# Kernel tuning notes

Measured on AMD Instinct MI355X. Metric: run time of the kernel, lower is better.

Reference implementation:

```python
import jax, jax.numpy as jnp
import numpy as np

B, N, D = 512, 120, 64
NB = 8  # n_freq_bands
S_CLIP, DELTA_CLIP = 10.0, 5.0


def zc_rms(x, g, eps=1e-8):
    # zero-centred RMS norm
    x0 = x - x0_mean(x)
    return x0 * jax.lax.rsqrt(jnp.mean(x0 * x0, axis=-1, keepdims=True) + eps) * g


def x0_mean(x):
    return jnp.mean(x, axis=-1, keepdims=True)


def l2norm(x, eps=1e-8):
    return x * jax.lax.rsqrt(jnp.sum(x * x, axis=-1, keepdims=True) + eps)


def setup_inputs() -> dict:
    key = jax.random.key(0)
    ks = jax.random.split(key, 12)
    s = 1.0 / np.sqrt(D)
    return {
        "x": jax.random.normal(ks[0], (B, N, D), dtype=jnp.float32),
        "g_norm": jnp.ones((D,), jnp.float32),
        "Wq": jax.random.normal(ks[1], (D, D), jnp.float32) * s,
        "Wk": jax.random.normal(ks[2], (D, D), jnp.float32) * s,
        "Wv": jax.random.normal(ks[3], (D, D), jnp.float32) * s,
        "bv": jnp.zeros((D,), jnp.float32),
        "Wo": jax.random.normal(ks[4], (D, D), jnp.float32) * s,
        "bo": jnp.zeros((D,), jnp.float32),
        "g_post": jnp.ones((D,), jnp.float32),
        "W1": jax.random.normal(ks[5], (NB, 16), jnp.float32) * (1.0 / np.sqrt(NB)),
        "b1": jnp.zeros((16,), jnp.float32),
        "W2": jax.random.normal(ks[6], (16, 1), jnp.float32) * 0.25,
        "b2": jnp.full((1,), 0.5, jnp.float32),  # bias init 0.5 as in torch
    }


def _gamma(h, W1, b1, W2, b2):
    # FFT over embedding dim, band-averaged energies -> gate in [0.5, 0.99]
    fft = jnp.abs(jnp.fft.rfft(jax.lax.stop_gradient(h), axis=-1))  # (B,N,n_f)
    n_f = fft.shape[-1]
    bs = max(1, n_f // NB)
    bands = [fft[..., i * bs:min(i * bs + bs, n_f)].mean(-1) for i in range(NB)]
    energy = jnp.stack(bands, axis=-1)  # (B,N,NB)
    energy = energy / jnp.clip(jnp.sum(energy, axis=-1, keepdims=True), 1e-8)
    hdn = jax.nn.silu(energy @ W1 + b1)
    raw = jax.nn.sigmoid(hdn @ W2 + b2)  # (B,N,1)
    return 0.5 + 0.49 * raw


def reference(x, g_norm, Wq, Wk, Wv, bv, Wo, bo, g_post, W1, b1, W2, b2):
    h = zc_rms(x, g_norm)
    q = l2norm(h @ Wq)
    k = l2norm(h @ Wk)
    v = h @ Wv + bv
    gamma = _gamma(h, W1, b1, W2, b2)  # (B,N,1)

    # time-major for scan
    qT = jnp.moveaxis(q, 1, 0)      # (N,B,D)
    kT = jnp.moveaxis(k, 1, 0)
    vT = jnp.moveaxis(v, 1, 0)
    gT = jnp.moveaxis(gamma, 1, 0)  # (N,B,1)

    S0 = jnp.zeros((x.shape[0], D, D), x.dtype)

    def step(S, inp):
        q_t, k_t, v_t, g_t = inp
        pred = jnp.einsum('bde,be->bd', S, k_t)
        delta = jnp.clip(v_t - pred, -DELTA_CLIP, DELTA_CLIP)
        S = g_t[..., None] * S + delta[:, :, None] * k_t[:, None, :]
        S = jnp.clip(S, -S_CLIP, S_CLIP)
        o_t = jnp.einsum('bde,be->bd', S, q_t)
        return S, o_t

    _, outT = jax.lax.scan(step, S0, (qT, kT, vT, gT))
    out = jnp.moveaxis(outT, 0, 1)  # (B,N,D)
    out = zc_rms(out, g_post) @ Wo + bo  # dropout is identity at inference
    return x + out
```

## Files before the change

kernel.cpp:

```cpp
#include <hip/hip_runtime.h>
#include <math.h>

#define B_ 512
#define N_ 120

typedef __attribute__((ext_vector_type(8))) _Float16 f16x8;
typedef __attribute__((ext_vector_type(2))) _Float16 f16x2;
typedef __attribute__((ext_vector_type(4))) float f32x4;
typedef __attribute__((ext_vector_type(2))) float f32x2;
typedef __attribute__((ext_vector_type(4))) int i32x4;

#define DPP_XOR1 0xB1
#define DPP_XOR2 0x4E
#define DPP_HMIR 0x141
#define DPP_MIR  0x140
template<int CTRL>
__device__ __forceinline__ float dpp_add(float v) {
    int x = __builtin_amdgcn_mov_dpp(__float_as_int(v), CTRL, 0xF, 0xF, true);
    return v + __int_as_float(x);
}

__device__ __forceinline__ float mix_lo(float a, int b, float c) {
    float d;
    asm("v_fma_mix_f32 %0, %1, %2, %3 op_sel:[0,0,0] op_sel_hi:[0,1,0]"
        : "=v"(d) : "v"(a), "v"(b), "v"(c));
    return d;
}
__device__ __forceinline__ float mix_hi(float a, int b, float c) {
    float d;
    asm("v_fma_mix_f32 %0, %1, %2, %3 op_sel:[0,1,0] op_sel_hi:[0,1,0]"
        : "=v"(d) : "v"(a), "v"(b), "v"(c));
    return d;
}
__device__ __forceinline__ f32x2 pk_mul2(f32x2 a, f32x2 b) {
    f32x2 d;
    asm("v_pk_mul_f32 %0, %1, %2" : "=v"(d) : "v"(a), "v"(b));
    return d;
}

#define OFF_WQ 0
#define OFF_WK 4096
#define OFF_WV 8192
#define OFF_T  12288
#define OFF_XF 16384
#define OFF_QS 0
#define OFF_KS 7680
#define OFF_VS 15360
#define OFF_OF 23040
#define OFF_WO 31232
#define LDS_F16 35328

__device__ __forceinline__ void mm4(f16x8 a0, f16x8 a1, const _Float16* wmat,
                                    int lane, f32x4* acc) {
    const f16x8* wv = (const f16x8*)wmat;
    #pragma unroll
    for (int nt = 0; nt < 4; ++nt) {
        f32x4 z = {0.f, 0.f, 0.f, 0.f};
        z = __builtin_amdgcn_mfma_f32_16x16x32_f16(a0, wv[nt * 128 + lane], z, 0, 0, 0);
        z = __builtin_amdgcn_mfma_f32_16x16x32_f16(a1, wv[nt * 128 + 64 + lane], z, 0, 0, 0);
        acc[nt] = z;
    }
}

__global__ __launch_bounds__(512, 4) void fused_kdn(
    const float* __restrict__ x, const float* __restrict__ g_norm,
    const float* __restrict__ Wq, const float* __restrict__ Wk,
    const float* __restrict__ Wv, const float* __restrict__ bv,
    const float* __restrict__ Wo, const float* __restrict__ bo,
    const float* __restrict__ g_post,
    const float* __restrict__ W1, const float* __restrict__ b1,
    const float* __restrict__ W2, const float* __restrict__ b2,
    float* out)
{
    __shared__ __align__(16) _Float16 L[LDS_F16];
    __shared__ __align__(16) float g_s[N_];
    __shared__ float bv_s[64], bo_s[64];
    __shared__ float sW1[128], sb1[16], sW2[16], sb2_s[1];

    int tid = threadIdx.x, wave = tid >> 6, lane = tid & 63;
    int b = blockIdx.x;

    if (tid < 128) sW1[tid] = W1[tid];
    if (tid >= 128 && tid < 144) sb1[tid - 128] = b1[tid - 128];
    if (tid >= 144 && tid < 160) sW2[tid - 144] = W2[tid - 144];
    if (tid == 160) sb2_s[0] = b2[0];
    if (tid >= 192 && tid < 256) bv_s[tid - 192] = bv[tid - 192];
    if (tid >= 256 && tid < 320) bo_s[tid - 256] = bo[tid - 256];
    if (tid < 128) {
        f16x8 z = {0, 0, 0, 0, 0, 0, 0, 0};
        *(f16x8*)&L[OFF_XF + 7168 + tid * 8] = z;
        *(f16x8*)&L[OFF_OF + 7168 + tid * 8] = z;
    }
    int sn = tid & 63, sk0 = (tid >> 6) * 8;
    int widx = (sn >> 4) * 1024 + (sk0 >> 5) * 512 + ((((sk0 >> 3) & 3) << 4) + (sn & 15)) * 8;
    {
        const float* Ws[4] = { Wq, Wk, Wv, Wo };
        const int woff[4] = { OFF_WQ, OFF_WK, OFF_WV, OFF_WO };
        #pragma unroll
        for (int m = 0; m < 4; ++m) {
            f16x8 pv;
            #pragma unroll
            for (int j = 0; j < 8; ++j) pv[j] = (_Float16)Ws[m][(sk0 + j) * 64 + sn];
            *(f16x8*)&L[woff[m] + widx] = pv;
        }
        f16x8 pv;
        int nn = sn & 31;
        #pragma unroll
        for (int j = 0; j < 8; ++j) {
            int kk = ((sk0 + j) * nn) & 63;
            float a = (float)kk * (6.283185307179586f / 64.0f);
            float s, c; __sincosf(a, &s, &c);
            pv[j] = (_Float16)((sn < 32) ? c : s);
        }
        *(f16x8*)&L[OFF_T + widx] = pv;
    }
    __syncthreads();

    const float* xb = x + (size_t)b * N_ * 64;
    float* ob_g = out + (size_t)b * N_ * 64;

    {
        float gn = g_norm[lane];
        int hbase = (lane >> 5) * 512 + ((lane >> 3) & 3) * 128 + (lane & 7);
        #pragma unroll 5
        for (int c = 0; c < 15; ++c) {
            int row = wave * 15 + c;
            float xv = xb[row * 64 + lane];
            float sx = xv, sxx = xv * xv;
            sx = dpp_add<DPP_XOR1>(sx); sxx = dpp_add<DPP_XOR1>(sxx);
            sx = dpp_add<DPP_XOR2>(sx); sxx = dpp_add<DPP_XOR2>(sxx);
            sx = dpp_add<DPP_HMIR>(sx); sxx = dpp_add<DPP_HMIR>(sxx);
            sx = dpp_add<DPP_MIR >(sx); sxx = dpp_add<DPP_MIR >(sxx);
            sx += __shfl_xor(sx, 16);   sxx += __shfl_xor(sxx, 16);
            sx += __shfl_xor(sx, 32);   sxx += __shfl_xor(sxx, 32);
            float mean = sx * 0.015625f;
            float var  = sxx * 0.015625f - mean * mean;
            float h = (xv - mean) * rsqrtf(var + 1e-8f) * gn;
            float hp = __shfl_xor(h, 1);
            if (!(lane & 1)) {
                f16x2 pk2 = { (_Float16)h, (_Float16)hp };
                *(f16x2*)&L[OFF_XF + (row >> 4) * 1024 + (row & 15) * 8 + hbase] = pk2;
            }
        }
    }
    __syncthreads();

    int grp = lane >> 4, li = lane & 15;
    int rbase = wave * 16 + grp * 4;
    {
        const f16x8* hfv = (const f16x8*)(L + OFF_XF);
        f16x8 a0 = hfv[wave * 128 + lane];
        f16x8 a1 = hfv[wave * 128 + 64 + lane];
        f32x4 accT[4];

        mm4(a0, a1, L + OFF_T, lane, accT);
        {
            int gb2 = lane & 48;
            #pragma unroll
            for (int reg = 0; reg < 4; ++reg) {
                float re1 = accT[0][reg], re2 = accT[1][reg];
                float im1 = accT[2][reg], im2 = accT[3][reg];
                float m1 = sqrtf(fmaf(re1, re1, im1 * im1));
                float m2 = sqrtf(fmaf(re2, re2, im2 * im2));
                m1 = dpp_add<DPP_XOR1>(m1); m2 = dpp_add<DPP_XOR1>(m2);
                m1 = dpp_add<DPP_XOR2>(m1); m2 = dpp_add<DPP_XOR2>(m2);
                float e1 = m1 * 0.25f, e2 = m2 * 0.25f;
                float tot = e1 + e2;
                tot = dpp_add<DPP_HMIR>(tot);
                tot = dpp_add<DPP_MIR >(tot);
                float rinv = 1.0f / fmaxf(tot, 1e-8f);
                float en1 = e1 * rinv, en2 = e2 * rinv;
                float hs = sb1[li];
                #pragma unroll
                for (int i = 0; i < 4; ++i)
                    hs = fmaf(__shfl(en1, gb2 + (i << 2)), sW1[i * 16 + li], hs);
                #pragma unroll
                for (int i = 0; i < 4; ++i)
                    hs = fmaf(__shfl(en2, gb2 + (i << 2)), sW1[(i + 4) * 16 + li], hs);
                float act = hs / (1.0f + __expf(-hs));
                float p = act * sW2[li];
                p = dpp_add<DPP_XOR1>(p);
                p = dpp_add<DPP_XOR2>(p);
                p = dpp_add<DPP_HMIR>(p);
                p = dpp_add<DPP_MIR >(p);
                float raw = 1.0f / (1.0f + __expf(-(p + sb2_s[0])));
                int row = rbase + reg;
                if (li == 0 && row < N_) g_s[row] = fmaf(0.49f, raw, 0.5f);
            }
        }

        f32x4 accq[4], acck[4], accv[4];
        mm4(a0, a1, L + OFF_WQ, lane, accq);
        mm4(a0, a1, L + OFF_WK, lane, acck);
        mm4(a0, a1, L + OFF_WV, lane, accv);

        {
            f32x4 sq = accq[0]*accq[0] + accq[1]*accq[1] + accq[2]*accq[2] + accq[3]*accq[3];
            f32x4 sk = acck[0]*acck[0] + acck[1]*acck[1] + acck[2]*acck[2] + acck[3]*acck[3];
            #pragma unroll
            for (int reg = 0; reg < 4; ++reg) {
                float qs = sq[reg], ks = sk[reg];
                qs = dpp_add<DPP_XOR1>(qs); ks = dpp_add<DPP_XOR1>(ks);
                qs = dpp_add<DPP_XOR2>(qs); ks = dpp_add<DPP_XOR2>(ks);
                qs = dpp_add<DPP_HMIR>(qs); ks = dpp_add<DPP_HMIR>(ks);
                qs = dpp_add<DPP_MIR >(qs); ks = dpp_add<DPP_MIR >(ks);
                float rq = rsqrtf(qs + 1e-8f), rk = rsqrtf(ks + 1e-8f);
                #pragma unroll
                for (int nt = 0; nt < 4; ++nt) { accq[nt][reg] *= rq; acck[nt][reg] *= rk; }
            }
            #pragma unroll
            for (int nt = 0; nt < 4; ++nt) {
                float bvn = bv_s[nt * 16 + li];
                #pragma unroll
                for (int reg = 0; reg < 4; ++reg) accv[nt][reg] += bvn;
            }
        }
        __syncthreads();

        #pragma unroll
        for (int reg = 0; reg < 4; ++reg) {
            int row = rbase + reg;
            if (row < N_) {
                int base = row * 64 + li;
                #pragma unroll
                for (int nt = 0; nt < 4; ++nt) {
                    L[OFF_QS + base + nt * 16] = (_Float16)accq[nt][reg];
                    L[OFF_KS + base + nt * 16] = (_Float16)acck[nt][reg];
                    L[OFF_VS + base + nt * 16] = (_Float16)accv[nt][reg];
                }
            }
        }
    }
    __syncthreads();

    {
        int g8 = lane & 7, dlo = lane >> 3;
        int d = wave * 8 + dlo;
        int co = g8 * 8;
        int dbase = (d >> 5) * 512 + ((d >> 3) & 3) * 128 + (d & 7);
        const _Float16* ks = L + OFF_KS;
        const _Float16* qs = L + OFF_QS;
        const _Float16* vp = L + OFF_VS + d;

        f32x2 S2[4];
        #pragma unroll
        for (int j = 0; j < 4; ++j) { S2[j].x = 0.f; S2[j].y = 0.f; }

        f16x8 kh = *(const f16x8*)&ks[co];
        f16x8 qh = *(const f16x8*)&qs[co];
        _Float16 vh = vp[0];
        f16x8 kn = *(const f16x8*)&ks[64 + co];
        f16x8 qn = *(const f16x8*)&qs[64 + co];
        _Float16 vn = vp[64];
        float pbc = 0.f;
        float4 gq = *(const float4*)&g_s[0];

#define PAIR(j, kh2, qh2, kn2) {                                               \
            f32x2 t2 = pk_mul2(gt2, S2[j]);                                    \
            float sA = mix_lo(delta, kh2, t2.x);                               \
            float sB = mix_hi(delta, kh2, t2.y);                               \
            sA = __builtin_amdgcn_fmed3f(sA, -10.f, 10.f);                     \
            sB = __builtin_amdgcn_fmed3f(sB, -10.f, 10.f);                     \
            S2[j].x = sA; S2[j].y = sB;                                        \
            oa = mix_lo(sA, qh2, oa);  ob = mix_hi(sB, qh2, ob);               \
            pa = mix_lo(sA, kn2, pa);  pb = mix_hi(sB, kn2, pb); }

#define SCAN_STEP(T, TF, GT)                                                   \
        {                                                                      \
            f16x8 kf = *(const f16x8*)&ks[(TF) * 64 + co];                     \
            f16x8 qf = *(const f16x8*)&qs[(TF) * 64 + co];                     \
            _Float16 vf = vp[(TF) * 64];                                       \
            float gt = (GT);                                                   \
            f32x2 gt2; gt2.x = gt; gt2.y = gt;                                 \
            float delta = __builtin_amdgcn_fmed3f((float)vh - pbc, -5.0f, 5.0f);\
            i32x4 khi = *(i32x4*)&kh;                                          \
            i32x4 qhi = *(i32x4*)&qh;                                          \
            i32x4 kni = *(i32x4*)&kn;                                          \
            float oa = 0.f, ob = 0.f, pa = 0.f, pb = 0.f;                      \
            PAIR(0, khi[0], qhi[0], kni[0])                                    \
            PAIR(1, khi[1], qhi[1], kni[1])                                    \
            PAIR(2, khi[2], qhi[2], kni[2])                                    \
            PAIR(3, khi[3], qhi[3], kni[3])                                    \
            float o = oa + ob;                                                 \
            o = dpp_add<DPP_XOR1>(o);                                          \
            o = dpp_add<DPP_XOR2>(o);                                          \
            o = dpp_add<DPP_HMIR>(o);                                          \
            float pn = pa + pb;                                                \
            pn = dpp_add<DPP_XOR1>(pn);                                        \
            pn = dpp_add<DPP_XOR2>(pn);                                        \
            pn = dpp_add<DPP_HMIR>(pn);                                        \
            if (g8 == 0)                                                       \
                L[OFF_OF + ((T) >> 4) * 1024 + ((T) & 15) * 8 + dbase] = (_Float16)o; \
            pbc = pn;                                                          \
            kh = kn; qh = qn; vh = vn;                                         \
            kn = kf; qn = qf; vn = vf;                                         \
        }

        for (int t4 = 0; t4 < 116; t4 += 4) {
            float4 gq_n = *(const float4*)&g_s[t4 + 4];
            SCAN_STEP(t4 + 0, t4 + 2, gq.x)
            SCAN_STEP(t4 + 1, t4 + 3, gq.y)
            SCAN_STEP(t4 + 2, t4 + 4, gq.z)
            SCAN_STEP(t4 + 3, t4 + 5, gq.w)
            gq = gq_n;
        }
        SCAN_STEP(116, 118, gq.x)
        SCAN_STEP(117, 119, gq.y)
        SCAN_STEP(118, 119, gq.z)
        SCAN_STEP(119, 119, gq.w)
#undef SCAN_STEP
#undef PAIR
    }
    __syncthreads();

    {
        float gp = g_post[lane];
        int hbase = (lane >> 5) * 512 + ((lane >> 3) & 3) * 128 + (lane & 7);
        #pragma unroll 5
        for (int c = 0; c < 15; ++c) {
            int row = wave * 15 + c;
            int ridx = OFF_OF + (row >> 4) * 1024 + (row & 15) * 8;
            float ov = (float)L[ridx + hbase];
            float sx = ov, sxx = ov * ov;
            sx = dpp_add<DPP_XOR1>(sx); sxx = dpp_add<DPP_XOR1>(sxx);
            sx = dpp_add<DPP_XOR2>(sx); sxx = dpp_add<DPP_XOR2>(sxx);
            sx = dpp_add<DPP_HMIR>(sx); sxx = dpp_add<DPP_HMIR>(sxx);
            sx = dpp_add<DPP_MIR >(sx); sxx = dpp_add<DPP_MIR >(sxx);
            sx += __shfl_xor(sx, 16);   sxx += __shfl_xor(sxx, 16);
            sx += __shfl_xor(sx, 32);   sxx += __shfl_xor(sxx, 32);
            float mean = sx * 0.015625f;
            float var  = sxx * 0.015625f - mean * mean;
            float hn = (ov - mean) * rsqrtf(var + 1e-8f) * gp;
            float hp = __shfl_xor(hn, 1);
            if (!(lane & 1)) {
                f16x2 pk2 = { (_Float16)hn, (_Float16)hp };
                *(f16x2*)&L[ridx + hbase] = pk2;
            }
        }
    }
    __syncthreads();

    {
        const f16x8* hfv = (const f16x8*)(L + OFF_OF);
        f16x8 a0 = hfv[wave * 128 + lane];
        f16x8 a1 = hfv[wave * 128 + 64 + lane];
        f32x4 acc[4];
        mm4(a0, a1, L + OFF_WO, lane, acc);
        #pragma unroll
        for (int reg = 0; reg < 4; ++reg) {
            int row = rbase + reg;
            if (row < N_) {
                #pragma unroll
                for (int nt = 0; nt < 4; ++nt) {
                    int idx = row * 64 + nt * 16 + li;
                    ob_g[idx] = acc[nt][reg] + bo_s[nt * 16 + li] + xb[idx];
                }
            }
        }
    }
}

extern "C" void kernel_launch(void* const* d_in, const int* in_sizes, int n_in,
                              void* d_out, int out_size, void* d_ws, size_t ws_size,
                              hipStream_t stream)
{
    const float* x      = (const float*)d_in[0];
    const float* g_norm = (const float*)d_in[1];
    const float* Wq     = (const float*)d_in[2];
    const float* Wk     = (const float*)d_in[3];
    const float* Wv     = (const float*)d_in[4];
    const float* bv     = (const float*)d_in[5];
    const float* Wo     = (const float*)d_in[6];
    const float* bo     = (const float*)d_in[7];
    const float* g_post = (const float*)d_in[8];
    const float* W1     = (const float*)d_in[9];
    const float* b1     = (const float*)d_in[10];
    const float* W2     = (const float*)d_in[11];
    const float* b2     = (const float*)d_in[12];
    float* out = (float*)d_out;

    fused_kdn<<<B_, 512, 0, stream>>>(x, g_norm, Wq, Wk, Wv, bv, Wo, bo, g_post,
                                      W1, b1, W2, b2, out);
}
```

Measured before the change: 157.8 us.

## Compute scan state-vector products with MFMA on four waves

The recurrent scan is restructured so the per-step matrix-vector products (S·q for the output and S·k_next for the next prediction) run as 16x16x32 MFMA instructions instead of per-lane mixed-precision FMAs followed by DPP reductions. The updated state is packed to fp16 each step and used as the A operand, with column 0 of B holding q and column 1 holding the next k. Only four waves run the scan, and deltas are exchanged through a small LDS scratch each step. This removes the cross-lane reduction chains but adds an LDS round-trip and MFMA latency on the serial critical path, halves scan parallelism, and rounds S to fp16 before the products.

```diff
diff --git a/kernel.cpp b/kernel.cpp
--- a/kernel.cpp
+++ b/kernel.cpp
@@ -36,6 +36,10 @@
     f32x2 d;
     asm("v_pk_mul_f32 %0, %1, %2" : "=v"(d) : "v"(a), "v"(b));
     return d;
+}
+__device__ __forceinline__ int pkrtz_i32(float a, float b) {
+    auto sp = __builtin_amdgcn_cvt_pkrtz(a, b);
+    return *(int*)&sp;
 }
 
 #define OFF_WQ 0
@@ -74,6 +78,7 @@
 {
     __shared__ __align__(16) _Float16 L[LDS_F16];
     __shared__ __align__(16) float g_s[N_];
+    __shared__ __align__(16) float dsc[4][16];
     __shared__ float bv_s[64], bo_s[64];
     __shared__ float sW1[128], sb1[16], sW2[16], sb2_s[1];
 
@@ -233,83 +238,83 @@
     }
     __syncthreads();
 
-    {
-        int g8 = lane & 7, dlo = lane >> 3;
-        int d = wave * 8 + dlo;
-        int co = g8 * 8;
-        int dbase = (d >> 5) * 512 + ((d >> 3) & 3) * 128 + (d & 7);
-        const _Float16* ks = L + OFF_KS;
-        const _Float16* qs = L + OFF_QS;
-        const _Float16* vp = L + OFF_VS + d;
-
-        f32x2 S2[4];
-        #pragma unroll
-        for (int j = 0; j < 4; ++j) { S2[j].x = 0.f; S2[j].y = 0.f; }
-
-        f16x8 kh = *(const f16x8*)&ks[co];
-        f16x8 qh = *(const f16x8*)&qs[co];
-        _Float16 vh = vp[0];
-        f16x8 kn = *(const f16x8*)&ks[64 + co];
-        f16x8 qn = *(const f16x8*)&qs[64 + co];
-        _Float16 vn = vp[64];
-        float pbc = 0.f;
+    if (wave < 4) {
+        int col = lane & 15;
+        int kg  = lane >> 4;
+        int c0  = kg * 8;
+        int d0  = wave * 16 + kg * 4;
+        int dpart = (d0 >> 5) * 512 + ((d0 >> 3) & 3) * 128 + (d0 & 7);
+        const _Float16* ksp = L + OFF_KS;
+        const _Float16* qsp = L + OFF_QS;
+        const _Float16* vsp = L + OFF_VS;
+        const _Float16* bbase = (col == 1) ? (ksp + 64 + c0) : (qsp + c0);
+
+        f32x2 S2[8];
+        #pragma unroll
+        for (int j = 0; j < 8; ++j) { S2[j].x = 0.f; S2[j].y = 0.f; }
+        f32x4 ppC = {0.f, 0.f, 0.f, 0.f};
+        const float fone = 1.0f, fzero = 0.0f;
         float4 gq = *(const float4*)&g_s[0];
 
-#define PAIR(j, kh2, qh2, kn2) {                                               \
+#define UPD2(j, KW, DST)                                                       \
+        {                                                                      \
             f32x2 t2 = pk_mul2(gt2, S2[j]);                                    \
-            float sA = mix_lo(delta, kh2, t2.x);                               \
-            float sB = mix_hi(delta, kh2, t2.y);                               \
-            sA = __builtin_amdgcn_fmed3f(sA, -10.f, 10.f);                     \
-            sB = __builtin_amdgcn_fmed3f(sB, -10.f, 10.f);                     \
-            S2[j].x = sA; S2[j].y = sB;                                        \
-            oa = mix_lo(sA, qh2, oa);  ob = mix_hi(sB, qh2, ob);               \
-            pa = mix_lo(sA, kn2, pa);  pb = mix_hi(sB, kn2, pb); }
-
-#define SCAN_STEP(T, TF, GT)                                                   \
+            float sa = mix_lo(delta, KW, t2.x);                                \
+            float sb = mix_hi(delta, KW, t2.y);                                \
+            sa = __builtin_amdgcn_fmed3f(sa, -10.f, 10.f);                     \
+            sb = __builtin_amdgcn_fmed3f(sb, -10.f, 10.f);                     \
+            S2[j].x = sa; S2[j].y = sb;                                        \
+            DST = pkrtz_i32(sa, sb);                                           \
+        }
+
+#define SCAN_IT(T, GT)                                                         \
         {                                                                      \
-            f16x8 kf = *(const f16x8*)&ks[(TF) * 64 + co];                     \
-            f16x8 qf = *(const f16x8*)&qs[(TF) * 64 + co];                     \
-            _Float16 vf = vp[(TF) * 64];                                       \
+            int2  vw  = *(const int2 *)&vsp[(T) * 64 + d0];                    \
+            f16x8 ku0 = *(const f16x8*)&ksp[(T) * 64 + c0];                    \
+            f16x8 ku1 = *(const f16x8*)&ksp[(T) * 64 + c0 + 32];               \
+            f16x8 b0  = *(const f16x8*)&bbase[(T) * 64];                       \
+            f16x8 b1  = *(const f16x8*)&bbase[(T) * 64 + 32];                  \
             float gt = (GT);                                                   \
             f32x2 gt2; gt2.x = gt; gt2.y = gt;                                 \
-            float delta = __builtin_amdgcn_fmed3f((float)vh - pbc, -5.0f, 5.0f);\
-            i32x4 khi = *(i32x4*)&kh;                                          \
-            i32x4 qhi = *(i32x4*)&qh;                                          \
-            i32x4 kni = *(i32x4*)&kn;                                          \
-            float oa = 0.f, ob = 0.f, pa = 0.f, pb = 0.f;                      \
-            PAIR(0, khi[0], qhi[0], kni[0])                                    \
-            PAIR(1, khi[1], qhi[1], kni[1])                                    \
-            PAIR(2, khi[2], qhi[2], kni[2])                                    \
-            PAIR(3, khi[3], qhi[3], kni[3])                                    \
-            float o = oa + ob;                                                 \
-            o = dpp_add<DPP_XOR1>(o);                                          \
-            o = dpp_add<DPP_XOR2>(o);                                          \
-            o = dpp_add<DPP_HMIR>(o);                                          \
-            float pn = pa + pb;                                                \
-            pn = dpp_add<DPP_XOR1>(pn);                                        \
-            pn = dpp_add<DPP_XOR2>(pn);                                        \
-            pn = dpp_add<DPP_HMIR>(pn);                                        \
-            if (g8 == 0)                                                       \
-                L[OFF_OF + ((T) >> 4) * 1024 + ((T) & 15) * 8 + dbase] = (_Float16)o; \
-            pbc = pn;                                                          \
-            kh = kn; qh = qn; vh = vn;                                         \
-            kn = kf; qn = qf; vn = vf;                                         \
-        }
-
-        for (int t4 = 0; t4 < 116; t4 += 4) {
-            float4 gq_n = *(const float4*)&g_s[t4 + 4];
-            SCAN_STEP(t4 + 0, t4 + 2, gq.x)
-            SCAN_STEP(t4 + 1, t4 + 3, gq.y)
-            SCAN_STEP(t4 + 2, t4 + 4, gq.z)
-            SCAN_STEP(t4 + 3, t4 + 5, gq.w)
+            f32x4 dr;                                                          \
+            dr[0] = __builtin_amdgcn_fmed3f(mix_lo(fone, vw.x, fzero) - ppC[0], -5.f, 5.f); \
+            dr[1] = __builtin_amdgcn_fmed3f(mix_hi(fone, vw.x, fzero) - ppC[1], -5.f, 5.f); \
+            dr[2] = __builtin_amdgcn_fmed3f(mix_lo(fone, vw.y, fzero) - ppC[2], -5.f, 5.f); \
+            dr[3] = __builtin_amdgcn_fmed3f(mix_hi(fone, vw.y, fzero) - ppC[3], -5.f, 5.f); \
+            if (col == 1) *(f32x4*)&dsc[wave][kg * 4] = dr;                    \
+            float delta = dsc[wave][col];                                      \
+            i32x4 k0i = *(i32x4*)&ku0;                                         \
+            i32x4 k1i = *(i32x4*)&ku1;                                         \
+            i32x4 a0i, a1i;                                                    \
+            UPD2(0, k0i[0], a0i[0]) UPD2(1, k0i[1], a0i[1])                    \
+            UPD2(2, k0i[2], a0i[2]) UPD2(3, k0i[3], a0i[3])                    \
+            UPD2(4, k1i[0], a1i[0]) UPD2(5, k1i[1], a1i[1])                    \
+            UPD2(6, k1i[2], a1i[2]) UPD2(7, k1i[3], a1i[3])                    \
+            f16x8 a0s = *(f16x8*)&a0i;                                         \
+            f16x8 a1s = *(f16x8*)&a1i;                                         \
+            f32x4 C = {0.f, 0.f, 0.f, 0.f};                                    \
+            C = __builtin_amdgcn_mfma_f32_16x16x32_f16(a0s, b0, C, 0, 0, 0);   \
+            C = __builtin_amdgcn_mfma_f32_16x16x32_f16(a1s, b1, C, 0, 0, 0);   \
+            if (col == 0) {                                                    \
+                f16x2 o01 = { (_Float16)C[0], (_Float16)C[1] };                \
+                f16x2 o23 = { (_Float16)C[2], (_Float16)C[3] };                \
+                int oidx = OFF_OF + (((T) >> 4) * 1024) + (((T) & 15) * 8) + dpart; \
+                *(f16x2*)&L[oidx]     = o01;                                   \
+                *(f16x2*)&L[oidx + 2] = o23;                                   \
+            }                                                                  \
+            ppC = C;                                                           \
+        }
+
+        for (int t4 = 0; t4 < N_; t4 += 4) {
+            float4 gq_n = (t4 + 4 < N_) ? *(const float4*)&g_s[t4 + 4] : gq;
+            SCAN_IT(t4 + 0, gq.x)
+            SCAN_IT(t4 + 1, gq.y)
+            SCAN_IT(t4 + 2, gq.z)
+            SCAN_IT(t4 + 3, gq.w)
             gq = gq_n;
         }
-        SCAN_STEP(116, 118, gq.x)
-        SCAN_STEP(117, 119, gq.y)
-        SCAN_STEP(118, 119, gq.z)
-        SCAN_STEP(119, 119, gq.w)
-#undef SCAN_STEP
-#undef PAIR
+#undef SCAN_IT
+#undef UPD2
     }
     __syncthreads();
 
```

Result: faster. 153.4 us (-2.8%).
